# Kernel tuning notes

Measured on AMD Instinct MI355X. Metric: run time of the kernel, lower is better.

## Reference

```python
import jax, jax.numpy as jnp
import numpy as np

B, S, D = 2, 2048, 2048
H, KVH = 32, 8
HD = D // H            # 64
G = H // KVH           # 4 kv groups
SCALE = 1.0 / np.sqrt(HD)


def setup_inputs() -> dict:
    key = jax.random.key(0)
    k1, k2, k3, k4, k5 = jax.random.split(key, 5)
    hidden_states = jax.random.normal(k1, (B, S, D), dtype=jnp.float32)
    Wq = jax.random.normal(k2, (D, H * HD), dtype=jnp.float32) * 0.02
    Wk = jax.random.normal(k3, (D, KVH * HD), dtype=jnp.float32) * 0.02
    Wv = jax.random.normal(k4, (D, KVH * HD), dtype=jnp.float32) * 0.02
    Wo = jax.random.normal(k5, (H * HD, D), dtype=jnp.float32) * 0.02
    return {"hidden_states": hidden_states, "Wq": Wq, "Wk": Wk, "Wv": Wv, "Wo": Wo}


def reference(hidden_states, Wq, Wk, Wv, Wo):
    B_, S_, _ = hidden_states.shape
    q = (hidden_states @ Wq).reshape(B_, S_, H, HD).transpose(0, 2, 1, 3)      # [B,H,S,HD]
    k = (hidden_states @ Wk).reshape(B_, S_, KVH, HD).transpose(0, 2, 1, 3)    # [B,KVH,S,HD]
    v = (hidden_states @ Wv).reshape(B_, S_, KVH, HD).transpose(0, 2, 1, 3)
    # repeat_interleave over head dim: kv head g serves q heads [g*G, (g+1)*G)
    k = jnp.repeat(k, G, axis=1)  # [B,H,S,HD]
    v = jnp.repeat(v, G, axis=1)
    scores = jnp.einsum('bhqd,bhkd->bhqk', q, k) * SCALE
    probs = jax.nn.softmax(scores.astype(jnp.float32), axis=-1).astype(q.dtype)
    # dropout is identity in eval mode
    out = jnp.einsum('bhqk,bhkd->bhqd', probs, v)             # [B,H,S,HD]
    out = out.transpose(0, 2, 1, 3).reshape(B_, S_, H * HD)   # [B,S,D]
    return out @ Wo
```

## Files before the change

kernel.cpp:

```cpp
#include <hip/hip_runtime.h>
#include <hip/hip_bf16.h>

typedef unsigned short u16;
typedef __attribute__((ext_vector_type(8))) short short8;
typedef __attribute__((ext_vector_type(4))) float f32x4;
typedef __attribute__((ext_vector_type(16))) float f32x16;
typedef __attribute__((ext_vector_type(4))) unsigned short u16x4;
typedef __attribute__((ext_vector_type(4))) int int4v;

#define S_LEN 2048
#define NH 32
#define NKV 8
#define QSCALE 0.18033688011112042f
#define PSHIFT 14.0f

__device__ __forceinline__ float fexp2(float x) { return __builtin_amdgcn_exp2f(x); }

__device__ __forceinline__ u16 f2bf(float f) {
  unsigned int u = __builtin_bit_cast(unsigned int, f);
  u += 0x7fffu + ((u >> 16) & 1u);
  return (u16)(u >> 16);
}

__device__ __forceinline__ unsigned int pk2bf(float a, float b) {
  float2 t; t.x = a; t.y = b;
  __hip_bfloat162 h = __float22bfloat162_rn(t);
  unsigned int r;
  __builtin_memcpy(&r, &h, 4);
  return r;
}

__device__ __forceinline__ void async16(const void* g, void* l) {
  __builtin_amdgcn_global_load_lds(
      (__attribute__((address_space(1))) void*)g,
      (__attribute__((address_space(3))) void*)l, 16, 0, 0);
}

__device__ __forceinline__ short8 mk_pf(unsigned a, unsigned b, unsigned c, unsigned d) {
  int4v t; t.x = (int)a; t.y = (int)b; t.z = (int)c; t.w = (int)d;
  return __builtin_bit_cast(short8, t);
}

__global__ __launch_bounds__(256) void prep_kernel(const float* __restrict__ X,
                                                   const float* __restrict__ Wq,
                                                   const float* __restrict__ Wk,
                                                   const float* __restrict__ Wv,
                                                   const float* __restrict__ Wo,
                                                   u16* __restrict__ Xb,
                                                   u16* __restrict__ Wqt,
                                                   u16* __restrict__ Wkt,
                                                   u16* __restrict__ Wvt,
                                                   u16* __restrict__ Wot) {
  __shared__ float tile[32][33];
  int bx = blockIdx.x, tid = threadIdx.x;
  if (bx < 8192) {
    int idx = bx * 256 + tid;
    float4 v = ((const float4*)X)[idx];
    u16x4 o;
    o.x = f2bf(v.x); o.y = f2bf(v.y); o.z = f2bf(v.z); o.w = f2bf(v.w);
    *(u16x4*)&Xb[(size_t)idx * 4] = o;
    return;
  }
  const float* in; u16* out; int N, bi;
  if (bx < 12288)      { bi = bx - 8192;  in = Wq; out = Wqt; N = 2048; }
  else if (bx < 13312) { bi = bx - 12288; in = Wk; out = Wkt; N = 512; }
  else if (bx < 14336) { bi = bx - 13312; in = Wv; out = Wvt; N = 512; }
  else                 { bi = bx - 14336; in = Wo; out = Wot; N = 2048; }
  const int K = 2048;
  int nbx = N >> 5;
  int n0 = (bi % nbx) * 32, k0 = (bi / nbx) * 32;
  int tx = tid & 31, ty = tid >> 5;
#pragma unroll
  for (int i = 0; i < 32; i += 8)
    tile[ty + i][tx] = in[(size_t)(k0 + ty + i) * N + n0 + tx];
  __syncthreads();
#pragma unroll
  for (int i = 0; i < 32; i += 8)
    out[(size_t)(n0 + ty + i) * K + k0 + tx] = f2bf(tile[tx][ty + i]);
}

__global__ __launch_bounds__(256) void gemm_qkv(const u16* __restrict__ A,
                                                const u16* __restrict__ Wqt,
                                                const u16* __restrict__ Wkvt,
                                                u16* __restrict__ Qb,
                                                u16* __restrict__ KVb) {
  __shared__ u16 la0[4096], la1[4096], lb0[4096], lb1[4096];
  int tid = threadIdx.x, bx = blockIdx.x;
  int mode, bm, bn;
  const u16* Bt;
  if (bx < 512) { mode = 0; bm = bx >> 4; bn = bx & 15; Bt = Wqt; }
  else          { mode = 1; int b2 = bx - 512; bm = b2 >> 3; bn = b2 & 7; Bt = Wkvt; }
  const int K = 2048;
  int w = tid >> 6, lane = tid & 63, qd = lane >> 4, ln = lane & 15;
  int wm = w >> 1, wn = w & 1;
  f32x4 acc[4][4];
#pragma unroll
  for (int i = 0; i < 4; ++i)
#pragma unroll
    for (int j = 0; j < 4; ++j) acc[i][j] = {0.f, 0.f, 0.f, 0.f};

  const u16* Ab = A + (size_t)bm * 128 * K;
  const u16* Bb = Bt + (size_t)bn * 128 * K;
  int row0 = tid >> 2, c0 = tid & 3;
  int g0 = c0 ^ (row0 & 3) ^ ((row0 >> 2) & 3);
  int s1 = tid + 256, row1 = s1 >> 2, c1 = s1 & 3;
  int g1 = c1 ^ (row1 & 3) ^ ((row1 >> 2) & 3);
  int pat = (ln & 3) ^ ((ln >> 2) & 3);
  int goff = (qd ^ pat) * 8;
  const u16* pa0 = Ab + (size_t)row0 * K + g0 * 8;
  const u16* pa1 = Ab + (size_t)row1 * K + g1 * 8;
  const u16* pb0 = Bb + (size_t)row0 * K + g0 * 8;
  const u16* pb1 = Bb + (size_t)row1 * K + g1 * 8;

#define QKV_STAGE(LA, LB, OFS)                      \
  async16(pa0 + (OFS), &LA[tid * 8]);               \
  async16(pa1 + (OFS), &LA[2048 + tid * 8]);        \
  async16(pb0 + (OFS), &LB[tid * 8]);               \
  async16(pb1 + (OFS), &LB[2048 + tid * 8]);

#define QKV_COMPUTE(LA, LB)                                                        \
  {                                                                                \
    short8 af[4], bf[4];                                                           \
    _Pragma("unroll") for (int i = 0; i < 4; ++i)                                  \
        af[i] = *(const short8*)&LA[(wm * 64 + i * 16 + ln) * 32 + goff];          \
    _Pragma("unroll") for (int j = 0; j < 4; ++j)                                  \
        bf[j] = *(const short8*)&LB[(wn * 64 + j * 16 + ln) * 32 + goff];          \
    __builtin_amdgcn_s_setprio(1);                                                 \
    _Pragma("unroll") for (int i = 0; i < 4; ++i)                                  \
      _Pragma("unroll") for (int j = 0; j < 4; ++j)                                \
        acc[i][j] =                                                                \
            __builtin_amdgcn_mfma_f32_16x16x32_bf16(af[i], bf[j], acc[i][j], 0, 0, 0); \
    __builtin_amdgcn_s_setprio(0);                                                 \
  }

  QKV_STAGE(la0, lb0, 0);
  __syncthreads();

  for (int kt = 0; kt < K; kt += 64) {
    QKV_STAGE(la1, lb1, kt + 32);
    QKV_COMPUTE(la0, lb0);
    __syncthreads();
    if (kt + 64 < K) { QKV_STAGE(la0, lb0, kt + 64); }
    QKV_COMPUTE(la1, lb1);
    __syncthreads();
  }
#undef QKV_STAGE
#undef QKV_COMPUTE

#pragma unroll
  for (int i = 0; i < 4; ++i)
#pragma unroll
    for (int r = 0; r < 4; ++r) {
      int m = bm * 128 + wm * 64 + i * 16 + qd * 4 + r;
      int b = m >> 11, s = m & 2047;
#pragma unroll
      for (int j = 0; j < 4; ++j) {
        int n = bn * 128 + wn * 64 + j * 16 + ln;
        float v = acc[i][j][r];
        int hh = n >> 6, hd = n & 63;
        if (mode == 0) {
          Qb[(((size_t)(b * NH + hh)) * S_LEN + s) * 64 + hd] = f2bf(v * QSCALE);
        } else {
          if (hh < 8)
            KVb[(((size_t)(b * NKV + hh)) * S_LEN + s) * 64 + hd] = f2bf(v);
          else
            KVb[2097152 + (((size_t)(b * NKV + (hh - 8))) * 64 + hd) * S_LEN + s] = f2bf(v);
        }
      }
    }
}

__global__ __launch_bounds__(256) void gemm_out(const u16* __restrict__ A,
                                                const u16* __restrict__ Bt,
                                                float* __restrict__ outp) {
  __shared__ u16 la0[4096], la1[4096], lb0[4096], lb1[4096];
  const int K = 2048, N = 2048;
  int tid = threadIdx.x;
  int bm = blockIdx.x >> 4, bn = blockIdx.x & 15;
  int w = tid >> 6, lane = tid & 63, qd = lane >> 4, ln = lane & 15;
  int wm = w >> 1, wn = w & 1;
  f32x4 acc[4][4];
#pragma unroll
  for (int i = 0; i < 4; ++i)
#pragma unroll
    for (int j = 0; j < 4; ++j) acc[i][j] = {0.f, 0.f, 0.f, 0.f};

  const u16* Ab = A + (size_t)bm * 128 * K;
  const u16* Bb = Bt + (size_t)bn * 128 * K;
  int row0 = tid >> 2, c0 = tid & 3;
  int g0 = c0 ^ (row0 & 3) ^ ((row0 >> 2) & 3);
  int s1 = tid + 256, row1 = s1 >> 2, c1 = s1 & 3;
  int g1 = c1 ^ (row1 & 3) ^ ((row1 >> 2) & 3);
  int pat = (ln & 3) ^ ((ln >> 2) & 3);
  int goff = (qd ^ pat) * 8;
  const u16* pa0 = Ab + (size_t)row0 * K + g0 * 8;
  const u16* pa1 = Ab + (size_t)row1 * K + g1 * 8;
  const u16* pb0 = Bb + (size_t)row0 * K + g0 * 8;
  const u16* pb1 = Bb + (size_t)row1 * K + g1 * 8;

#define OUT_STAGE(LA, LB, OFS)                      \
  async16(pa0 + (OFS), &LA[tid * 8]);               \
  async16(pa1 + (OFS), &LA[2048 + tid * 8]);        \
  async16(pb0 + (OFS), &LB[tid * 8]);               \
  async16(pb1 + (OFS), &LB[2048 + tid * 8]);

#define OUT_COMPUTE(LA, LB)                                                        \
  {                                                                                \
    short8 af[4], bf[4];                                                           \
    _Pragma("unroll") for (int i = 0; i < 4; ++i)                                  \
        af[i] = *(const short8*)&LA[(wm * 64 + i * 16 + ln) * 32 + goff];          \
    _Pragma("unroll") for (int j = 0; j < 4; ++j)                                  \
        bf[j] = *(const short8*)&LB[(wn * 64 + j * 16 + ln) * 32 + goff];          \
    __builtin_amdgcn_s_setprio(1);                                                 \
    _Pragma("unroll") for (int i = 0; i < 4; ++i)                                  \
      _Pragma("unroll") for (int j = 0; j < 4; ++j)                                \
        acc[i][j] =                                                                \
            __builtin_amdgcn_mfma_f32_16x16x32_bf16(af[i], bf[j], acc[i][j], 0, 0, 0); \
    __builtin_amdgcn_s_setprio(0);                                                 \
  }

  OUT_STAGE(la0, lb0, 0);
  __syncthreads();

  for (int kt = 0; kt < K; kt += 64) {
    OUT_STAGE(la1, lb1, kt + 32);
    OUT_COMPUTE(la0, lb0);
    __syncthreads();
    if (kt + 64 < K) { OUT_STAGE(la0, lb0, kt + 64); }
    OUT_COMPUTE(la1, lb1);
    __syncthreads();
  }
#undef OUT_STAGE
#undef OUT_COMPUTE

#pragma unroll
  for (int i = 0; i < 4; ++i)
#pragma unroll
    for (int r = 0; r < 4; ++r) {
      int m = bm * 128 + wm * 64 + i * 16 + qd * 4 + r;
#pragma unroll
      for (int j = 0; j < 4; ++j) {
        int n = bn * 128 + wn * 64 + j * 16 + ln;
        outp[(size_t)m * N + n] = acc[i][j][r];
      }
    }
}

__global__ __launch_bounds__(256) void attn_kernel(const u16* __restrict__ Q,
                                                   const u16* __restrict__ K,
                                                   const u16* __restrict__ VT,
                                                   u16* __restrict__ Ao) {
  __shared__ u16 lds_k[2][4096];
  __shared__ u16 lds_v[2][4096];
  int tid = threadIdx.x;
  int w = tid >> 6, lane = tid & 63;
  int l31 = lane & 31, l5 = lane >> 5;
  int qt = blockIdx.x & 15, bh = blockIdx.x >> 4;
  int b = bh >> 5, h = bh & 31, g = h >> 2;
  const u16* gQ = Q + ((size_t)bh * S_LEN + qt * 128) * 64;
  const u16* gK = K + (size_t)(b * NKV + g) * S_LEN * 64;
  const u16* gV = VT + (size_t)(b * NKV + g) * 64 * S_LEN;

  int p7 = l31 & 7;

  int s0 = tid, r0 = s0 >> 3, c0 = s0 & 7, gg0 = c0 ^ (r0 & 7);
  int s1 = tid + 256, r1 = s1 >> 3, c1 = s1 & 7, gg1 = c1 ^ (r1 & 7);

  u16* qstage = &lds_k[0][0];
#pragma unroll
  for (int k = 0; k < 4; ++k) {
    int s = tid + k * 256;
    int q = s >> 3, c = s & 7, gg = c ^ (q & 7);
    async16(gQ + (size_t)q * 64 + gg * 8, &qstage[s * 8]);
  }
  __syncthreads();
  short8 qf[4];
  int qrow = w * 32 + l31;
#pragma unroll
  for (int ks = 0; ks < 4; ++ks)
    qf[ks] = *(const short8*)&qstage[qrow * 64 + ((ks * 2 + l5) ^ p7) * 8];
  __syncthreads();

  async16(gK + (size_t)r0 * 64 + gg0 * 8, &lds_k[0][s0 * 8]);
  async16(gK + (size_t)r1 * 64 + gg1 * 8, &lds_k[0][s1 * 8]);
  async16(gV + (size_t)r0 * S_LEN + gg0 * 8, &lds_v[0][s0 * 8]);
  async16(gV + (size_t)r1 * S_LEN + gg1 * 8, &lds_v[0][s1 * 8]);

  const f32x16 psh16 = {-PSHIFT, -PSHIFT, -PSHIFT, -PSHIFT, -PSHIFT, -PSHIFT,
                        -PSHIFT, -PSHIFT, -PSHIFT, -PSHIFT, -PSHIFT, -PSHIFT,
                        -PSHIFT, -PSHIFT, -PSHIFT, -PSHIFT};
  f32x16 accO[2];
#pragma unroll
  for (int hb = 0; hb < 2; ++hb)
#pragma unroll
    for (int t = 0; t < 16; ++t) accO[hb][t] = 0.f;
  float li = 0.f;

  for (int c = 0; c < 32; ++c) {
    int cur = c & 1;
    if (c < 31) {
      int nb = cur ^ 1, cn = c + 1;
      async16(gK + (size_t)(cn * 64 + r0) * 64 + gg0 * 8, &lds_k[nb][s0 * 8]);
      async16(gK + (size_t)(cn * 64 + r1) * 64 + gg1 * 8, &lds_k[nb][s1 * 8]);
      async16(gV + (size_t)r0 * S_LEN + cn * 64 + gg0 * 8, &lds_v[nb][s0 * 8]);
      async16(gV + (size_t)r1 * S_LEN + cn * 64 + gg1 * 8, &lds_v[nb][s1 * 8]);
    }
    const u16* kb = lds_k[cur];
    const u16* vb = lds_v[cur];

#pragma unroll
    for (int kblk = 0; kblk < 2; ++kblk) {
      f32x16 sc = psh16;
      __builtin_amdgcn_s_setprio(1);
#pragma unroll
      for (int ks = 0; ks < 4; ++ks) {
        short8 kf = *(const short8*)&kb[(kblk * 32 + l31) * 64 + ((ks * 2 + l5) ^ p7) * 8];
        sc = __builtin_amdgcn_mfma_f32_32x32x16_bf16(kf, qf[ks], sc, 0, 0, 0);
      }
      __builtin_amdgcn_s_setprio(0);

      float p[16];
#pragma unroll
      for (int t = 0; t < 16; ++t) p[t] = fexp2(sc[t]);
#pragma unroll
      for (int t = 0; t < 16; t += 4) li += (p[t] + p[t + 1]) + (p[t + 2] + p[t + 3]);
      unsigned W[8];
#pragma unroll
      for (int t = 0; t < 8; ++t) W[t] = pk2bf(p[2 * t], p[2 * t + 1]);
      auto ra = __builtin_amdgcn_permlane32_swap((int)W[0], (int)W[2], false, false);
      auto rb = __builtin_amdgcn_permlane32_swap((int)W[1], (int)W[3], false, false);
      auto rc = __builtin_amdgcn_permlane32_swap((int)W[4], (int)W[6], false, false);
      auto rd = __builtin_amdgcn_permlane32_swap((int)W[5], (int)W[7], false, false);
      short8 pf0 = mk_pf((unsigned)ra[0], (unsigned)rb[0], (unsigned)ra[1], (unsigned)rb[1]);
      short8 pf1 = mk_pf((unsigned)rc[0], (unsigned)rd[0], (unsigned)rc[1], (unsigned)rd[1]);

      __builtin_amdgcn_s_setprio(1);
#pragma unroll
      for (int hb = 0; hb < 2; ++hb) {
        short8 vf = *(const short8*)&vb[(hb * 32 + l31) * 64 + ((kblk * 4 + l5) ^ p7) * 8];
        accO[hb] = __builtin_amdgcn_mfma_f32_32x32x16_bf16(vf, pf0, accO[hb], 0, 0, 0);
      }
#pragma unroll
      for (int hb = 0; hb < 2; ++hb) {
        short8 vf = *(const short8*)&vb[(hb * 32 + l31) * 64 + ((kblk * 4 + 2 + l5) ^ p7) * 8];
        accO[hb] = __builtin_amdgcn_mfma_f32_32x32x16_bf16(vf, pf1, accO[hb], 0, 0, 0);
      }
      __builtin_amdgcn_s_setprio(0);
    }
    __syncthreads();
  }

  float l = li + __shfl_xor(li, 32);
  float inv = 1.f / l;
  int q = qt * 128 + w * 32 + l31;
  size_t base = ((size_t)b * S_LEN + q) * 2048 + h * 64;
#pragma unroll
  for (int hb = 0; hb < 2; ++hb)
#pragma unroll
    for (int rq = 0; rq < 4; ++rq) {
      u16x4 o;
#pragma unroll
      for (int rr = 0; rr < 4; ++rr) o[rr] = f2bf(accO[hb][rq * 4 + rr] * inv);
      *(u16x4*)&Ao[base + hb * 32 + rq * 8 + l5 * 4] = o;
    }
}

extern "C" void kernel_launch(void* const* d_in, const int* in_sizes, int n_in,
                              void* d_out, int out_size, void* d_ws, size_t ws_size,
                              hipStream_t stream) {
  const float* X  = (const float*)d_in[0];
  const float* Wq = (const float*)d_in[1];
  const float* Wk = (const float*)d_in[2];
  const float* Wv = (const float*)d_in[3];
  const float* Wo = (const float*)d_in[4];
  char* ws = (char*)d_ws;
  u16* Xb  = (u16*)(ws);
  u16* Wqt = (u16*)(ws + 16777216);
  u16* Wkt = (u16*)(ws + 25165824);
  u16* Wvt = (u16*)(ws + 27262976);
  u16* Wot = (u16*)(ws + 29360128);
  u16* Qb  = (u16*)(ws + 37748736);
  u16* Kb  = (u16*)(ws + 54525952);
  u16* VTb = (u16*)(ws + 58720256);
  u16* Ab  = (u16*)(ws + 62914560);
  float* out = (float*)d_out;

  prep_kernel<<<18432, 256, 0, stream>>>(X, Wq, Wk, Wv, Wo, Xb, Wqt, Wkt, Wvt, Wot);
  gemm_qkv<<<768, 256, 0, stream>>>(Xb, Wqt, Wkt, Qb, Kb);
  attn_kernel<<<1024, 256, 0, stream>>>(Qb, Kb, VTb, Ab);
  gemm_out<<<512, 256, 0, stream>>>(Ab, Wot, out);
}
```

Before: 324.1 us.

## Process two 32-row query groups per wave to reuse K/V tiles

```diff
diff --git a/kernel.cpp b/kernel.cpp
--- a/kernel.cpp
+++ b/kernel.cpp
@@ -246,18 +246,17 @@
     }
 }
 
-__global__ __launch_bounds__(256) void attn_kernel(const u16* __restrict__ Q,
-                                                   const u16* __restrict__ K,
-                                                   const u16* __restrict__ VT,
-                                                   u16* __restrict__ Ao) {
-  __shared__ u16 lds_k[2][4096];
-  __shared__ u16 lds_v[2][4096];
+__global__ __launch_bounds__(256, 2) void attn_kernel(const u16* __restrict__ Q,
+                                                      const u16* __restrict__ K,
+                                                      const u16* __restrict__ VT,
+                                                      u16* __restrict__ Ao) {
+  __shared__ u16 sh[16384];
   int tid = threadIdx.x;
   int w = tid >> 6, lane = tid & 63;
   int l31 = lane & 31, l5 = lane >> 5;
-  int qt = blockIdx.x & 15, bh = blockIdx.x >> 4;
+  int qt = blockIdx.x & 7, bh = blockIdx.x >> 3;
   int b = bh >> 5, h = bh & 31, g = h >> 2;
-  const u16* gQ = Q + ((size_t)bh * S_LEN + qt * 128) * 64;
+  const u16* gQ = Q + ((size_t)bh * S_LEN + qt * 256) * 64;
   const u16* gK = K + (size_t)(b * NKV + g) * S_LEN * 64;
   const u16* gV = VT + (size_t)(b * NKV + g) * 64 * S_LEN;
 
@@ -266,103 +265,144 @@
   int s0 = tid, r0 = s0 >> 3, c0 = s0 & 7, gg0 = c0 ^ (r0 & 7);
   int s1 = tid + 256, r1 = s1 >> 3, c1 = s1 & 7, gg1 = c1 ^ (r1 & 7);
 
-  u16* qstage = &lds_k[0][0];
-#pragma unroll
-  for (int k = 0; k < 4; ++k) {
+#pragma unroll
+  for (int k = 0; k < 8; ++k) {
     int s = tid + k * 256;
     int q = s >> 3, c = s & 7, gg = c ^ (q & 7);
-    async16(gQ + (size_t)q * 64 + gg * 8, &qstage[s * 8]);
-  }
-  __syncthreads();
-  short8 qf[4];
-  int qrow = w * 32 + l31;
-#pragma unroll
-  for (int ks = 0; ks < 4; ++ks)
-    qf[ks] = *(const short8*)&qstage[qrow * 64 + ((ks * 2 + l5) ^ p7) * 8];
-  __syncthreads();
-
-  async16(gK + (size_t)r0 * 64 + gg0 * 8, &lds_k[0][s0 * 8]);
-  async16(gK + (size_t)r1 * 64 + gg1 * 8, &lds_k[0][s1 * 8]);
-  async16(gV + (size_t)r0 * S_LEN + gg0 * 8, &lds_v[0][s0 * 8]);
-  async16(gV + (size_t)r1 * S_LEN + gg1 * 8, &lds_v[0][s1 * 8]);
+    async16(gQ + (size_t)q * 64 + gg * 8, &sh[s * 8]);
+  }
+  __syncthreads();
+  short8 qf[2][4];
+#pragma unroll
+  for (int qg = 0; qg < 2; ++qg) {
+    int qrow = w * 64 + qg * 32 + l31;
+#pragma unroll
+    for (int ks = 0; ks < 4; ++ks)
+      qf[qg][ks] = *(const short8*)&sh[qrow * 64 + ((ks * 2 + l5) ^ p7) * 8];
+  }
+  __syncthreads();
+
+  async16(gK + (size_t)r0 * 64 + gg0 * 8, &sh[s0 * 8]);
+  async16(gK + (size_t)r1 * 64 + gg1 * 8, &sh[s1 * 8]);
+  async16(gV + (size_t)r0 * S_LEN + gg0 * 8, &sh[8192 + s0 * 8]);
+  async16(gV + (size_t)r1 * S_LEN + gg1 * 8, &sh[8192 + s1 * 8]);
+  __syncthreads();
 
   const f32x16 psh16 = {-PSHIFT, -PSHIFT, -PSHIFT, -PSHIFT, -PSHIFT, -PSHIFT,
                         -PSHIFT, -PSHIFT, -PSHIFT, -PSHIFT, -PSHIFT, -PSHIFT,
                         -PSHIFT, -PSHIFT, -PSHIFT, -PSHIFT};
-  f32x16 accO[2];
-#pragma unroll
-  for (int hb = 0; hb < 2; ++hb)
-#pragma unroll
-    for (int t = 0; t < 16; ++t) accO[hb][t] = 0.f;
-  float li = 0.f;
+  f32x16 accA0, accA1, accB0, accB1;
+#pragma unroll
+  for (int t = 0; t < 16; ++t) { accA0[t] = 0.f; accA1[t] = 0.f; accB0[t] = 0.f; accB1[t] = 0.f; }
+  float liA = 0.f, liB = 0.f;
+
+#define SOFTMAX32(SC, LI, PF0, PF1)                                              \
+  short8 PF0, PF1;                                                               \
+  {                                                                              \
+    float p[16];                                                                 \
+    _Pragma("unroll") for (int t = 0; t < 16; ++t) p[t] = fexp2(SC[t]);          \
+    _Pragma("unroll") for (int t = 0; t < 16; t += 4)                            \
+        LI += (p[t] + p[t + 1]) + (p[t + 2] + p[t + 3]);                         \
+    unsigned W[8];                                                               \
+    _Pragma("unroll") for (int t = 0; t < 8; ++t) W[t] = pk2bf(p[2 * t], p[2 * t + 1]); \
+    auto ra = __builtin_amdgcn_permlane32_swap((int)W[0], (int)W[2], false, false); \
+    auto rb = __builtin_amdgcn_permlane32_swap((int)W[1], (int)W[3], false, false); \
+    auto rc = __builtin_amdgcn_permlane32_swap((int)W[4], (int)W[6], false, false); \
+    auto rd = __builtin_amdgcn_permlane32_swap((int)W[5], (int)W[7], false, false); \
+    PF0 = mk_pf((unsigned)ra[0], (unsigned)rb[0], (unsigned)ra[1], (unsigned)rb[1]); \
+    PF1 = mk_pf((unsigned)rc[0], (unsigned)rd[0], (unsigned)rc[1], (unsigned)rd[1]); \
+  }
 
   for (int c = 0; c < 32; ++c) {
     int cur = c & 1;
     if (c < 31) {
       int nb = cur ^ 1, cn = c + 1;
-      async16(gK + (size_t)(cn * 64 + r0) * 64 + gg0 * 8, &lds_k[nb][s0 * 8]);
-      async16(gK + (size_t)(cn * 64 + r1) * 64 + gg1 * 8, &lds_k[nb][s1 * 8]);
-      async16(gV + (size_t)r0 * S_LEN + cn * 64 + gg0 * 8, &lds_v[nb][s0 * 8]);
-      async16(gV + (size_t)r1 * S_LEN + cn * 64 + gg1 * 8, &lds_v[nb][s1 * 8]);
-    }
-    const u16* kb = lds_k[cur];
-    const u16* vb = lds_v[cur];
+      async16(gK + (size_t)(cn * 64 + r0) * 64 + gg0 * 8, &sh[nb * 4096 + s0 * 8]);
+      async16(gK + (size_t)(cn * 64 + r1) * 64 + gg1 * 8, &sh[nb * 4096 + s1 * 8]);
+      async16(gV + (size_t)r0 * S_LEN + cn * 64 + gg0 * 8, &sh[8192 + nb * 4096 + s0 * 8]);
+      async16(gV + (size_t)r1 * S_LEN + cn * 64 + gg1 * 8, &sh[8192 + nb * 4096 + s1 * 8]);
+    }
+    const u16* kb = &sh[cur * 4096];
+    const u16* vb = &sh[8192 + cur * 4096];
 
 #pragma unroll
     for (int kblk = 0; kblk < 2; ++kblk) {
-      f32x16 sc = psh16;
+      f32x16 scA = psh16, scB = psh16;
       __builtin_amdgcn_s_setprio(1);
 #pragma unroll
       for (int ks = 0; ks < 4; ++ks) {
         short8 kf = *(const short8*)&kb[(kblk * 32 + l31) * 64 + ((ks * 2 + l5) ^ p7) * 8];
-        sc = __builtin_amdgcn_mfma_f32_32x32x16_bf16(kf, qf[ks], sc, 0, 0, 0);
+        scA = __builtin_amdgcn_mfma_f32_32x32x16_bf16(kf, qf[0][ks], scA, 0, 0, 0);
+        scB = __builtin_amdgcn_mfma_f32_32x32x16_bf16(kf, qf[1][ks], scB, 0, 0, 0);
       }
       __builtin_amdgcn_s_setprio(0);
 
-      float p[16];
-#pragma unroll
-      for (int t = 0; t < 16; ++t) p[t] = fexp2(sc[t]);
-#pragma unroll
-      for (int t = 0; t < 16; t += 4) li += (p[t] + p[t + 1]) + (p[t + 2] + p[t + 3]);
-      unsigned W[8];
-#pragma unroll
-      for (int t = 0; t < 8; ++t) W[t] = pk2bf(p[2 * t], p[2 * t + 1]);
-      auto ra = __builtin_amdgcn_permlane32_swap((int)W[0], (int)W[2], false, false);
-      auto rb = __builtin_amdgcn_permlane32_swap((int)W[1], (int)W[3], false, false);
-      auto rc = __builtin_amdgcn_permlane32_swap((int)W[4], (int)W[6], false, false);
-      auto rd = __builtin_amdgcn_permlane32_swap((int)W[5], (int)W[7], false, false);
-      short8 pf0 = mk_pf((unsigned)ra[0], (unsigned)rb[0], (unsigned)ra[1], (unsigned)rb[1]);
-      short8 pf1 = mk_pf((unsigned)rc[0], (unsigned)rd[0], (unsigned)rc[1], (unsigned)rd[1]);
+      SOFTMAX32(scA, liA, pfA0, pfA1)
+      SOFTMAX32(scB, liB, pfB0, pfB1)
 
       __builtin_amdgcn_s_setprio(1);
 #pragma unroll
       for (int hb = 0; hb < 2; ++hb) {
         short8 vf = *(const short8*)&vb[(hb * 32 + l31) * 64 + ((kblk * 4 + l5) ^ p7) * 8];
-        accO[hb] = __builtin_amdgcn_mfma_f32_32x32x16_bf16(vf, pf0, accO[hb], 0, 0, 0);
+        if (hb == 0) {
+          accA0 = __builtin_amdgcn_mfma_f32_32x32x16_bf16(vf, pfA0, accA0, 0, 0, 0);
+          accB0 = __builtin_amdgcn_mfma_f32_32x32x16_bf16(vf, pfB0, accB0, 0, 0, 0);
+        } else {
+          accA1 = __builtin_amdgcn_mfma_f32_32x32x16_bf16(vf, pfA0, accA1, 0, 0, 0);
+          accB1 = __builtin_amdgcn_mfma_f32_32x32x16_bf16(vf, pfB0, accB1, 0, 0, 0);
+        }
       }
 #pragma unroll
       for (int hb = 0; hb < 2; ++hb) {
         short8 vf = *(const short8*)&vb[(hb * 32 + l31) * 64 + ((kblk * 4 + 2 + l5) ^ p7) * 8];
-        accO[hb] = __builtin_amdgcn_mfma_f32_32x32x16_bf16(vf, pf1, accO[hb], 0, 0, 0);
+        if (hb == 0) {
+          accA0 = __builtin_amdgcn_mfma_f32_32x32x16_bf16(vf, pfA1, accA0, 0, 0, 0);
+          accB0 = __builtin_amdgcn_mfma_f32_32x32x16_bf16(vf, pfB1, accB0, 0, 0, 0);
+        } else {
+          accA1 = __builtin_amdgcn_mfma_f32_32x32x16_bf16(vf, pfA1, accA1, 0, 0, 0);
+          accB1 = __builtin_amdgcn_mfma_f32_32x32x16_bf16(vf, pfB1, accB1, 0, 0, 0);
+        }
       }
       __builtin_amdgcn_s_setprio(0);
     }
     __syncthreads();
   }
-
-  float l = li + __shfl_xor(li, 32);
-  float inv = 1.f / l;
-  int q = qt * 128 + w * 32 + l31;
-  size_t base = ((size_t)b * S_LEN + q) * 2048 + h * 64;
-#pragma unroll
-  for (int hb = 0; hb < 2; ++hb)
+#undef SOFTMAX32
+
+  {
+    float l = liA + __shfl_xor(liA, 32);
+    float inv = 1.f / l;
+    int q = qt * 256 + w * 64 + l31;
+    size_t base = ((size_t)b * S_LEN + q) * 2048 + h * 64;
 #pragma unroll
     for (int rq = 0; rq < 4; ++rq) {
-      u16x4 o;
-#pragma unroll
-      for (int rr = 0; rr < 4; ++rr) o[rr] = f2bf(accO[hb][rq * 4 + rr] * inv);
-      *(u16x4*)&Ao[base + hb * 32 + rq * 8 + l5 * 4] = o;
-    }
+      u16x4 o0, o1;
+#pragma unroll
+      for (int rr = 0; rr < 4; ++rr) {
+        o0[rr] = f2bf(accA0[rq * 4 + rr] * inv);
+        o1[rr] = f2bf(accA1[rq * 4 + rr] * inv);
+      }
+      *(u16x4*)&Ao[base + rq * 8 + l5 * 4] = o0;
+      *(u16x4*)&Ao[base + 32 + rq * 8 + l5 * 4] = o1;
+    }
+  }
+  {
+    float l = liB + __shfl_xor(liB, 32);
+    float inv = 1.f / l;
+    int q = qt * 256 + w * 64 + 32 + l31;
+    size_t base = ((size_t)b * S_LEN + q) * 2048 + h * 64;
+#pragma unroll
+    for (int rq = 0; rq < 4; ++rq) {
+      u16x4 o0, o1;
+#pragma unroll
+      for (int rr = 0; rr < 4; ++rr) {
+        o0[rr] = f2bf(accB0[rq * 4 + rr] * inv);
+        o1[rr] = f2bf(accB1[rq * 4 + rr] * inv);
+      }
+      *(u16x4*)&Ao[base + rq * 8 + l5 * 4] = o0;
+      *(u16x4*)&Ao[base + 32 + rq * 8 + l5 * 4] = o1;
+    }
+  }
 }
 
 extern "C" void kernel_launch(void* const* d_in, const int* in_sizes, int n_in,
@@ -387,6 +427,6 @@
 
   prep_kernel<<<18432, 256, 0, stream>>>(X, Wq, Wk, Wv, Wo, Xb, Wqt, Wkt, Wvt, Wot);
   gemm_qkv<<<768, 256, 0, stream>>>(Xb, Wqt, Wkt, Qb, Kb);
-  attn_kernel<<<1024, 256, 0, stream>>>(Qb, Kb, VTb, Ab);
+  attn_kernel<<<512, 256, 0, stream>>>(Qb, Kb, VTb, Ab);
   gemm_out<<<512, 256, 0, stream>>>(Ab, Wot, out);
 }
```

After: 304.0 us. 6.2% less time.
